# Optimization experiments

Measured on AMD Instinct MI355X. Metric: run time of the kernel, lower is better.

Reference implementation:

```python
import jax, jax.numpy as jnp
import numpy as np

N_SAMPLES = 2 ** 15          # 32768
STEP = 256                   # transform_step_size
WIN = 2048                   # transform/synthesis window
N_FRAMES = N_SAMPLES // STEP # 128
N_COEFFS = WIN // 2 + 1      # 1025
DILATIONS = (1, 2, 4, 8, 16, 32, 64, 1)


def hann(n):
    return 0.5 - 0.5 * jnp.cos(2.0 * jnp.pi * jnp.arange(n, dtype=jnp.float32) / n)


def transform(audio):
    # audio: (B, 1, N) -> magnitude STFT (B, 1024, 128)
    x = audio[:, 0, :]
    x = jnp.pad(x, ((0, 0), (0, WIN - STEP)))  # pad so n_frames == N_SAMPLES // STEP
    idx = np.arange(N_FRAMES)[:, None] * STEP + np.arange(WIN)[None, :]
    frames = x[:, idx] * hann(WIN)
    spec = jnp.abs(jnp.fft.rfft(frames, norm='ortho'))   # (B, F, 1025)
    return spec[..., : N_COEFFS - 1].transpose(0, 2, 1)  # (B, 1024, F)


def conv1x1(x, w, b):
    # x: (B, I, T), w: (O, I, 1), b: (O,)
    return jnp.einsum('oi,bit->bot', w[:, :, 0], x) + b[None, :, None]


def anticausal_block(x, w, b, dilation):
    # kernel_size=2 anti-causal dilated conv: looks at t and t+dilation (pad future)
    x_fut = jnp.pad(x, ((0, 0), (0, 0), (0, dilation)))[:, :, dilation:]
    y = (jnp.einsum('oi,bit->bot', w[:, :, 0], x)
         + jnp.einsum('oi,bit->bot', w[:, :, 1], x_fut)
         + b[None, :, None])
    y = jax.nn.leaky_relu(y, 0.2)
    y = y + x
    # do_norm: per-example max-norm
    y = y / (jnp.max(jnp.abs(y), axis=(1, 2), keepdims=True) + 1e-8)
    return y


def upsample_with_holes(x, desired_size):
    # zero-stuffing upsample: out[..., ::step] = x
    b, c, t = x.shape
    step = desired_size // t
    out = jnp.zeros((b, c, desired_size), x.dtype)
    return out.at[:, :, ::step].set(x)


def freq_domain_resonance(coeffs):
    # coeffs: (1, C, 1025) in [0, 1); per-frame decay = repeated spectral multiply
    c = jnp.clip(coeffs, 0.0, 0.9999)
    exps = jnp.arange(1, N_FRAMES + 1, dtype=coeffs.dtype)
    mags = c[:, :, None, :] ** exps[None, None, :, None]     # (1, C, F, 1025)
    frames = jnp.fft.irfft(mags, n=WIN) * hann(WIN)
    hop = WIN // 2
    total = hop * (N_FRAMES - 1) + WIN
    idx = np.arange(N_FRAMES)[:, None] * hop + np.arange(WIN)[None, :]
    out = jnp.zeros(frames.shape[:2] + (total,), frames.dtype)
    out = out.at[:, :, idx].add(frames)                      # overlap-add
    return out[..., :N_SAMPLES]                              # (1, C, N)


def fft_convolve(a, b):
    # circular-free conv via zero-padding to 2N, keep first N (matches repo fft_convolve)
    n = a.shape[-1]
    spec = jnp.fft.rfft(a, n=2 * n) * jnp.fft.rfft(b, n=2 * n)
    return jnp.fft.irfft(spec, n=2 * n)[..., :n]


def reference(audio, proj_in_w, proj_in_b, blocks_w, blocks_b,
              proj_sparse_w, proj_sparse_b, proj_dense_w, proj_dense_b, resonances):
    spec = transform(audio)                         # (B, 1024, 128)
    h = conv1x1(spec, proj_in_w, proj_in_b)         # (B, 32, 128)
    acc = jnp.zeros_like(h)
    for i, d in enumerate(DILATIONS):               # fixed 8-block stack
        h = anticausal_block(h, blocks_w[i], blocks_b[i], d)
        acc = acc + h
    x = conv1x1(acc, proj_sparse_w, proj_sparse_b)  # (B, 256, 128)
    sparse = jax.nn.relu(x)
    x = conv1x1(sparse, proj_dense_w, proj_dense_b) # (B, 32, 128)
    x = upsample_with_holes(x, N_SAMPLES)           # (B, 32, 32768)
    res = freq_domain_resonance(resonances)         # (1, 32, 32768), broadcast over B
    y = fft_convolve(x, res)                        # (B, 32, 32768)
    y = jnp.sum(y, axis=1, keepdims=True)           # (B, 1, 32768)
    return y, sparse


def setup_inputs() -> dict:
    key = jax.random.key(0)
    ks = jax.random.split(key, 12)
    u = lambda k, shape: jax.random.uniform(k, shape, jnp.float32, -0.05, 0.05)
    return {
        'audio': jax.random.normal(ks[0], (32, 1, N_SAMPLES), jnp.float32),
        'proj_in_w': u(ks[1], (32, 1024, 1)),
        'proj_in_b': jnp.zeros((32,), jnp.float32),
        'blocks_w': u(ks[2], (8, 32, 32, 2)),
        'blocks_b': jnp.zeros((8, 32), jnp.float32),
        'proj_sparse_w': u(ks[3], (256, 32, 1)),
        'proj_sparse_b': jnp.zeros((256,), jnp.float32),
        'proj_dense_w': u(ks[4], (32, 256, 1)),
        'proj_dense_b': jnp.zeros((32,), jnp.float32),
        'resonances': jax.random.uniform(ks[5], (1, 32, N_COEFFS), jnp.float32, 0.0, 1.0),
    }
```

## Files before the change

kernel.cpp:

```cpp
#include <hip/hip_runtime.h>

#define PI_F 3.14159265358979323846f

typedef short bf16x8 __attribute__((ext_vector_type(8)));
typedef float f32x4 __attribute__((ext_vector_type(4)));

#define MFMA16(acc, a, b) \
  acc = __builtin_amdgcn_mfma_f32_16x16x32_bf16(a, b, acc, 0, 0, 0)

#define WS_SPEC   0u
#define WS_H0     4194304u
#define WS_ACC    4325376u
#define WS_V      4456448u
#define WS_WTIN   4587520u
#define WS_WST    4620288u
#define WS_WDT    4628480u
#define WS_FRAMES 4636672u
#define WS_RES    6733824u

__device__ __forceinline__ void fft2048_stages(float2* buf, int tid) {
  for (int stage = 0; stage < 11; ++stage) {
    int half = 1 << stage;
    float base = -PI_F / (float)half;
    for (int t = tid; t < 1024; t += 256) {
      int j  = t & (half - 1);
      int i0 = ((t >> stage) << (stage + 1)) + j;
      int i1 = i0 + half;
      float s, c;
      __sincosf(base * (float)j, &s, &c);
      float2 u = buf[i0];
      float2 w = buf[i1];
      float tr = c * w.x - s * w.y;
      float ti = c * w.y + s * w.x;
      buf[i0] = make_float2(u.x + tr, u.y + ti);
      buf[i1] = make_float2(u.x - tr, u.y - ti);
    }
    __syncthreads();
  }
}

__global__ __launch_bounds__(256) void k_fft(const float* __restrict__ audio,
                                             const float* __restrict__ resin,
                                             float* __restrict__ spec,
                                             float* __restrict__ frames) {
  __shared__ float2 buf[2048];
  int blk = blockIdx.x;
  if (blk < 2048) {
    int b  = blk >> 6;
    int f0 = (blk & 63) * 2;
    for (int j = threadIdx.x; j < 2048; j += 256) {
      float h = 0.5f - 0.5f * __cosf(0.0030679615757712823f * (float)j);
      int i1 = f0 * 256 + j;
      int i2 = i1 + 256;
      float a1 = (i1 < 32768) ? audio[b * 32768 + i1] : 0.f;
      float a2 = (i2 < 32768) ? audio[b * 32768 + i2] : 0.f;
      buf[__brev((unsigned)j) >> 21] = make_float2(a1 * h, a2 * h);
    }
    __syncthreads();
    fft2048_stages(buf, threadIdx.x);
    const float scale = 0.5f * 0.022097086912079608f;
    for (int k = threadIdx.x; k < 1024; k += 256) {
      float2 zk = buf[k];
      float2 zn = buf[(2048 - k) & 2047];
      float f1r = zk.x + zn.x, f1i = zk.y - zn.y;
      float f2r = zk.y + zn.y, f2i = zk.x - zn.x;
      spec[(b * 128 + f0) * 1024 + k]     = sqrtf(f1r * f1r + f1i * f1i) * scale;
      spec[(b * 128 + f0 + 1) * 1024 + k] = sqrtf(f2r * f2r + f2i * f2i) * scale;
    }
  } else {
    int r = blk - 2048;
    int c = r >> 4;
    int g = r & 15;
    float e1 = (float)(2 * g + 1);
    for (int k = threadIdx.x; k < 2048; k += 256) {
      int kk = (k <= 1024) ? k : 2048 - k;
      float cv = resin[c * 1025 + kk];
      cv = fminf(fmaxf(cv, 0.f), 0.9999f);
      float m1 = __powf(cv, e1);
      float m2 = m1 * cv;
      buf[__brev((unsigned)k) >> 21] = make_float2(m1, m2);
    }
    __syncthreads();
    fft2048_stages(buf, threadIdx.x);
    for (int j = threadIdx.x; j < 2048; j += 256) {
      float h  = 0.5f - 0.5f * __cosf(0.0030679615757712823f * (float)j);
      float sc = h * (1.f / 2048.f);
      float2 z = buf[j];
      frames[(c * 32 + 2 * g) * 2048 + j]     = z.x * sc;
      frames[(c * 32 + 2 * g + 1) * 2048 + j] = z.y * sc;
    }
  }
}

__global__ __launch_bounds__(256) void k_prep(const float* __restrict__ Win,
                                              const float* __restrict__ Ws,
                                              const float* __restrict__ Wd,
                                              const float* __restrict__ bwIn,
                                              float* __restrict__ WT,
                                              float* __restrict__ WsT,
                                              float* __restrict__ WdT,
                                              short* __restrict__ Whg,
                                              short* __restrict__ Wlg) {
  int i = blockIdx.x * 256 + threadIdx.x;
  if (i < 32768) { int o = i >> 10, k = i & 1023; WT[k * 32 + o] = Win[i]; }
  if (i < 8192)  { int o2 = i >> 5, m = i & 31;   WsT[m * 256 + o2] = Ws[i]; }
  if (i < 8192)  { int c = i >> 8, o2 = i & 255;  WdT[o2 * 32 + c] = Wd[i]; }
  if (i < 16384) {
    int w = i & 1, m = (i >> 1) & 31, o = (i >> 6) & 31, s = i >> 11;
    float val = bwIn[i];
    unsigned bits = __float_as_uint(val);
    float rem = val - __uint_as_float(bits & 0xffff0000u);
    int row = (s * 2 + w) * 32 + o;
    Whg[row * 32 + m] = (short)(bits >> 16);
    Wlg[row * 32 + m] = (short)(__float_as_uint(rem) >> 16);
  }
}

__global__ __launch_bounds__(256) void k_proj_in(const float* __restrict__ spec,
                                                 const float* __restrict__ WT,
                                                 const float* __restrict__ bias,
                                                 float* __restrict__ h0) {
  __shared__ float specL[8][1024];
  __shared__ float red[32][8][8];
  int b  = blockIdx.x >> 4;
  int t0 = (blockIdx.x & 15) * 8;
  for (int i = threadIdx.x; i < 8192; i += 256) {
    int tt = i >> 10, k = i & 1023;
    specL[tt][k] = spec[(b * 128 + t0 + tt) * 1024 + k];
  }
  __syncthreads();
  int o = threadIdx.x & 31, p = threadIdx.x >> 5;
  float part[8] = {0.f,0.f,0.f,0.f,0.f,0.f,0.f,0.f};
  for (int i = 0; i < 128; ++i) {
    int k = p * 128 + ((i + p * 4) & 127);
    float w = WT[k * 32 + o];
#pragma unroll
    for (int tt = 0; tt < 8; ++tt) part[tt] += w * specL[tt][k];
  }
#pragma unroll
  for (int tt = 0; tt < 8; ++tt) red[o][tt][p] = part[tt];
  __syncthreads();
  int oo = threadIdx.x >> 3, tt2 = threadIdx.x & 7;
  float s = bias[oo];
#pragma unroll
  for (int p2 = 0; p2 < 8; ++p2) s += red[oo][tt2][p2];
  h0[b * 4096 + oo * 128 + t0 + tt2] = s;
}

__global__ __launch_bounds__(1024) void k_chain(const float* __restrict__ h0,
                                                const short* __restrict__ Whg,
                                                const short* __restrict__ Wlg,
                                                const float* __restrict__ bb,
                                                float* __restrict__ accout) {
  __shared__ __align__(16) short Hh[192 * 40];
  __shared__ __align__(16) short Hl[192 * 40];
  __shared__ float Hf[128 * 33];
  __shared__ float bL[256];
  __shared__ float red[16];
  int b = blockIdx.x, tid = threadIdx.x;

  for (int i = tid; i < 4096; i += 1024) {
    int t = i & 127;
    int o = i >> 7;
    float val = h0[b * 4096 + i];
    Hf[t * 33 + o] = val;
    unsigned bits = __float_as_uint(val);
    float rem = val - __uint_as_float(bits & 0xffff0000u);
    Hh[t * 40 + o] = (short)(bits >> 16);
    Hl[t * 40 + o] = (short)(__float_as_uint(rem) >> 16);
  }
  for (int i = tid; i < 64 * 40; i += 1024) {
    Hh[128 * 40 + i] = 0;
    Hl[128 * 40 + i] = 0;
  }
  if (tid < 256) bL[tid] = bb[tid];
  __syncthreads();

  int wave = tid >> 6, lane = tid & 63;
  int quad = lane >> 4, l15 = lane & 15;
  int t0 = (wave & 7) * 16, o0 = (wave >> 3) * 16;
  int tD = t0 + quad * 4;
  int oD = o0 + l15;

  const bf16x8* Hh8 = (const bf16x8*)Hh;
  const bf16x8* Hl8 = (const bf16x8*)Hl;
  const bf16x8* Wh8 = (const bf16x8*)Whg;
  const bf16x8* Wl8 = (const bf16x8*)Wlg;

  float accsum[4] = {0.f, 0.f, 0.f, 0.f};
  const int DIL[8] = {1, 2, 4, 8, 16, 32, 64, 1};

#pragma unroll
  for (int s = 0; s < 8; ++s) {
    int arow = t0 + l15;
    int frow = arow + DIL[s];
    bf16x8 Ah = Hh8[arow * 5 + quad];
    bf16x8 Al = Hl8[arow * 5 + quad];
    bf16x8 Fh = Hh8[frow * 5 + quad];
    bf16x8 Fl = Hl8[frow * 5 + quad];
    int w0row = ((s * 2 + 0) * 32 + oD) * 4 + quad;
    int w1row = ((s * 2 + 1) * 32 + oD) * 4 + quad;
    bf16x8 B0h = Wh8[w0row], B0l = Wl8[w0row];
    bf16x8 B1h = Wh8[w1row], B1l = Wl8[w1row];
    float bias = bL[s * 32 + oD];
    f32x4 acc = {bias, bias, bias, bias};
    MFMA16(acc, Ah, B0h); MFMA16(acc, Ah, B0l); MFMA16(acc, Al, B0h);
    MFMA16(acc, Fh, B1h); MFMA16(acc, Fh, B1l); MFMA16(acc, Fl, B1h);
    float hnew[4], lmax = 0.f;
#pragma unroll
    for (int r = 0; r < 4; ++r) {
      float sv = acc[r];
      sv = (sv > 0.f) ? sv : 0.2f * sv;
      sv += Hf[(tD + r) * 33 + oD];
      hnew[r] = sv;
      lmax = fmaxf(lmax, fabsf(sv));
    }
#pragma unroll
    for (int off = 32; off > 0; off >>= 1)
      lmax = fmaxf(lmax, __shfl_down(lmax, off, 64));
    if (lane == 0) red[wave] = lmax;
    __syncthreads();
    float mx = red[0];
#pragma unroll
    for (int i = 1; i < 16; ++i) mx = fmaxf(mx, red[i]);
    float nm = 1.f / (mx + 1e-8f);
#pragma unroll
    for (int r = 0; r < 4; ++r) {
      float hv = hnew[r] * nm;
      accsum[r] += hv;
      int t = tD + r;
      Hf[t * 33 + oD] = hv;
      unsigned bits = __float_as_uint(hv);
      float rem = hv - __uint_as_float(bits & 0xffff0000u);
      Hh[t * 40 + oD] = (short)(bits >> 16);
      Hl[t * 40 + oD] = (short)(__float_as_uint(rem) >> 16);
    }
    __syncthreads();
  }
#pragma unroll
  for (int r = 0; r < 4; ++r)
    accout[b * 4096 + (tD + r) * 32 + oD] = accsum[r];
}

__global__ __launch_bounds__(256) void k_sparse_dense(const float* __restrict__ acc,
                                                      const float* __restrict__ WsT,
                                                      const float* __restrict__ bs,
                                                      const float* __restrict__ WdT,
                                                      const float* __restrict__ bd,
                                                      float* __restrict__ out_sparse,
                                                      float* __restrict__ v) {
  __shared__ float accL[32];
  __shared__ float sL[256];
  __shared__ float red[8][32];
  int b = blockIdx.x >> 7, t = blockIdx.x & 127;
  int tid = threadIdx.x;
  if (tid < 32) accL[tid] = acc[b * 4096 + t * 32 + tid];
  __syncthreads();
  float s = bs[tid];
  for (int m = 0; m < 32; ++m) s += WsT[m * 256 + tid] * accL[m];
  s = fmaxf(s, 0.f);
  out_sparse[b * 32768 + tid * 128 + t] = s;
  sL[tid] = s;
  __syncthreads();
  int c = tid & 31, p = tid >> 5;
  float part = 0.f;
  for (int j = 0; j < 32; ++j) {
    int o2 = p * 32 + j;
    part += WdT[o2 * 32 + c] * sL[o2];
  }
  red[p][c] = part;
  __syncthreads();
  if (tid < 32) {
    float vv = bd[tid];
    for (int p2 = 0; p2 < 8; ++p2) vv += red[p2][tid];
    v[b * 4096 + tid * 128 + t] = vv;
  }
}

__global__ __launch_bounds__(256) void k_res_assemble(const float* __restrict__ frames,
                                                      float* __restrict__ res) {
  int i = blockIdx.x * 256 + threadIdx.x;
  int c = i >> 15, s = i & 32767;
  int g = s >> 10, j0 = s & 1023;
  float v = frames[(c * 32 + g) * 2048 + j0];
  if (g > 0) v += frames[(c * 32 + g - 1) * 2048 + j0 + 1024];
  res[i] = v;
}

__global__ __launch_bounds__(256) void k_bpack(const float* __restrict__ res,
                                               short* __restrict__ Bh,
                                               short* __restrict__ Bl) {
  int c = blockIdx.x >> 4, o = blockIdx.x & 15;
  int r = threadIdx.x;
  bf16x8 hv, lv;
#pragma unroll
  for (int j = 0; j < 8; ++j) {
    float val = res[c * 32768 + (8 * o + j) * 256 + r];
    unsigned bits = __float_as_uint(val);
    float rem = val - __uint_as_float(bits & 0xffff0000u);
    hv[j] = (short)(bits >> 16);
    lv[j] = (short)(__float_as_uint(rem) >> 16);
  }
  int unit = (blockIdx.x * 16 + (r >> 4)) * 16 + (r & 15);
  ((bf16x8*)Bh)[unit] = hv;
  ((bf16x8*)Bl)[unit] = lv;
}

__global__ __launch_bounds__(256) void k_conv(const float* __restrict__ v,
                                              const short* __restrict__ Bh,
                                              const short* __restrict__ Bl,
                                              float* __restrict__ y) {
  __shared__ float vwin[32][33];
  __shared__ __align__(16) short Ah[16 * 520];
  __shared__ __align__(16) short Al[16 * 520];
  int blk = blockIdx.x;
  int b = blk / 36;
  int p = blk - b * 36;
  int qt = (int)((sqrtf(8.f * (float)p + 1.f) - 1.f) * 0.5f + 1e-4f);
  int uc = p - ((qt * (qt + 1)) >> 1);
  int q0 = qt * 16, u0 = uc * 16;
  int D0 = q0 - u0;

  for (int i = threadIdx.x; i < 1024; i += 256) {
    int c = i >> 5, ii = i & 31;
    int d = D0 - 15 + ii;
    vwin[c][ii] = (d >= 0 && d < 128) ? v[b * 4096 + c * 128 + d] : 0.f;
  }
  __syncthreads();
  for (int idx = threadIdx.x; idx < 8192; idx += 256) {
    int m = idx >> 9, kk = idx & 511;
    float val = vwin[kk >> 4][(m - (kk & 15)) + 15];
    unsigned bits = __float_as_uint(val);
    float rem = val - __uint_as_float(bits & 0xffff0000u);
    Ah[m * 520 + kk] = (short)(bits >> 16);
    Al[m * 520 + kk] = (short)(__float_as_uint(rem) >> 16);
  }
  __syncthreads();

  int lane = threadIdx.x & 63, wave = threadIdx.x >> 6;
  int quad = lane >> 4, l15 = lane & 15;
  int nt0 = wave * 4;

  f32x4 acc[4];
#pragma unroll
  for (int i = 0; i < 4; ++i) acc[i] = (f32x4)0.f;

  const bf16x8* Ah8 = (const bf16x8*)Ah;
  const bf16x8* Al8 = (const bf16x8*)Al;
  const bf16x8* Bh8 = (const bf16x8*)Bh;
  const bf16x8* Bl8 = (const bf16x8*)Bl;
  int aoff = l15 * 65 + quad;
  int og   = 2 * uc + (quad & 1);
  int cq   = quad >> 1;

#pragma unroll
  for (int ks = 0; ks < 16; ++ks) {
    bf16x8 avh = Ah8[aoff + 4 * ks];
    bf16x8 avl = Al8[aoff + 4 * ks];
    int c = 2 * ks + cq;
    int bbase = (c * 16 + og) * 256 + l15;
#pragma unroll
    for (int t = 0; t < 4; ++t) {
      int bi = bbase + (nt0 + t) * 16;
      bf16x8 bvh = Bh8[bi];
      bf16x8 bvl = Bl8[bi];
      MFMA16(acc[t], avh, bvh);
      MFMA16(acc[t], avh, bvl);
      MFMA16(acc[t], avl, bvh);
    }
  }

  float* yb = y + b * 32768 + (q0 + quad * 4) * 256 + l15;
#pragma unroll
  for (int t = 0; t < 4; ++t)
#pragma unroll
    for (int reg = 0; reg < 4; ++reg)
      atomicAdd(yb + reg * 256 + (nt0 + t) * 16, acc[t][reg]);
}

extern "C" void kernel_launch(void* const* d_in, const int* in_sizes, int n_in,
                              void* d_out, int out_size, void* d_ws, size_t ws_size,
                              hipStream_t stream) {
  const float* audio = (const float*)d_in[0];
  const float* Win   = (const float*)d_in[1];
  const float* bin   = (const float*)d_in[2];
  const float* bw    = (const float*)d_in[3];
  const float* bb    = (const float*)d_in[4];
  const float* Ws    = (const float*)d_in[5];
  const float* bs    = (const float*)d_in[6];
  const float* Wd    = (const float*)d_in[7];
  const float* bd    = (const float*)d_in[8];
  const float* reson = (const float*)d_in[9];

  float* out = (float*)d_out;
  float* ws  = (float*)d_ws;

  float* spec   = ws + WS_SPEC;
  float* h0     = ws + WS_H0;
  float* accb   = ws + WS_ACC;
  float* vbuf   = ws + WS_V;
  float* WT     = ws + WS_WTIN;
  float* WsT    = ws + WS_WST;
  float* WdT    = ws + WS_WDT;
  float* frames = ws + WS_FRAMES;
  float* resbuf = ws + WS_RES;
  short* Bh = (short*)(ws + WS_FRAMES);
  short* Bl = (short*)(ws + WS_FRAMES + 524288u);
  short* Whg = (short*)(ws + WS_V);
  short* Wlg = (short*)(ws + WS_V + 8192u);

  hipMemsetAsync(d_out, 0, 1048576u * sizeof(float), stream);

  k_prep<<<128, 256, 0, stream>>>(Win, Ws, Wd, bw, WT, WsT, WdT, Whg, Wlg);
  k_fft<<<2560, 256, 0, stream>>>(audio, reson, spec, frames);
  k_res_assemble<<<4096, 256, 0, stream>>>(frames, resbuf);
  k_bpack<<<512, 256, 0, stream>>>(resbuf, Bh, Bl);
  k_proj_in<<<512, 256, 0, stream>>>(spec, WT, bin, h0);
  k_chain<<<32, 1024, 0, stream>>>(h0, Whg, Wlg, bb, accb);
  k_sparse_dense<<<4096, 256, 0, stream>>>(accb, WsT, bs, WdT, bd, out + 1048576, vbuf);
  k_conv<<<1152, 256, 0, stream>>>(vbuf, Bh, Bl, out);
}
```

Baseline: 209.3 us.

## Enlarge k_conv tiles to reuse B fragments across two batches and two row tiles

Rewrites the bf16-split MFMA convolution kernel so each block handles two batch items and a 32-row output tile, with four A sub-tiles sharing every loaded B fragment. Channels are processed in two passes through a smaller Toeplitz A buffer in LDS. This cuts global B traffic and the number of atomic-add blocks, shrinking the grid from 1152 to 320 blocks. In exchange it raises register pressure (16 accumulators) and may hurt occupancy and load balance on the triangular tile schedule.

```diff
diff --git a/kernel.cpp b/kernel.cpp
--- a/kernel.cpp
+++ b/kernel.cpp
@@ -306,76 +306,118 @@
   ((bf16x8*)Bl)[unit] = lv;
 }
 
-__global__ __launch_bounds__(256) void k_conv(const float* __restrict__ v,
-                                              const short* __restrict__ Bh,
-                                              const short* __restrict__ Bl,
-                                              float* __restrict__ y) {
-  __shared__ float vwin[32][33];
-  __shared__ __align__(16) short Ah[16 * 520];
-  __shared__ __align__(16) short Al[16 * 520];
+__global__ __launch_bounds__(256, 2) void k_conv(const float* __restrict__ v,
+                                                 const short* __restrict__ Bh,
+                                                 const short* __restrict__ Bl,
+                                                 float* __restrict__ y) {
+  __shared__ __align__(16) short AH[2 * 32 * 264];
+  __shared__ __align__(16) short AL[2 * 32 * 264];
+  __shared__ float vwin[2][2][16][48];
+
   int blk = blockIdx.x;
-  int b = blk / 36;
-  int p = blk - b * 36;
-  int qt = (int)((sqrtf(8.f * (float)p + 1.f) - 1.f) * 0.5f + 1e-4f);
-  int uc = p - ((qt * (qt + 1)) >> 1);
-  int q0 = qt * 16, u0 = uc * 16;
-  int D0 = q0 - u0;
-
-  for (int i = threadIdx.x; i < 1024; i += 256) {
-    int c = i >> 5, ii = i & 31;
-    int d = D0 - 15 + ii;
-    vwin[c][ii] = (d >= 0 && d < 128) ? v[b * 4096 + c * 128 + d] : 0.f;
-  }
-  __syncthreads();
-  for (int idx = threadIdx.x; idx < 8192; idx += 256) {
-    int m = idx >> 9, kk = idx & 511;
-    float val = vwin[kk >> 4][(m - (kk & 15)) + 15];
-    unsigned bits = __float_as_uint(val);
-    float rem = val - __uint_as_float(bits & 0xffff0000u);
-    Ah[m * 520 + kk] = (short)(bits >> 16);
-    Al[m * 520 + kk] = (short)(__float_as_uint(rem) >> 16);
+  int b2 = blk / 20;
+  int e  = blk - b2 * 20;
+  int j, uc;
+  if      (e < 2)  { j = 0; uc = e; }
+  else if (e < 6)  { j = 1; uc = e - 2; }
+  else if (e < 12) { j = 2; uc = e - 6; }
+  else             { j = 3; uc = e - 12; }
+  int D0 = 32 * j - 16 * uc;
+
+  for (int i = threadIdx.x; i < 3008; i += 256) {
+    int ii = i % 47;
+    int r  = i / 47;
+    int c  = r & 15, p = (r >> 4) & 1, bbv = r >> 5;
+    int d  = D0 - 15 + ii;
+    vwin[bbv][p][c][ii] = (d >= 0 && d < 128)
+        ? v[(2 * b2 + bbv) * 4096 + (16 * p + c) * 128 + d] : 0.f;
   }
   __syncthreads();
 
   int lane = threadIdx.x & 63, wave = threadIdx.x >> 6;
   int quad = lane >> 4, l15 = lane & 15;
-  int nt0 = wave * 4;
-
-  f32x4 acc[4];
-#pragma unroll
-  for (int i = 0; i < 4; ++i) acc[i] = (f32x4)0.f;
-
-  const bf16x8* Ah8 = (const bf16x8*)Ah;
-  const bf16x8* Al8 = (const bf16x8*)Al;
+  int cq   = quad >> 1;
+  int og   = 2 * uc + (quad & 1);
+  int nt0  = wave * 4;
+
+  f32x4 acc[4][4];
+#pragma unroll
+  for (int a = 0; a < 4; ++a)
+#pragma unroll
+    for (int t = 0; t < 4; ++t) acc[a][t] = (f32x4)0.f;
+
+  const bf16x8* AH8 = (const bf16x8*)AH;
+  const bf16x8* AL8 = (const bf16x8*)AL;
   const bf16x8* Bh8 = (const bf16x8*)Bh;
   const bf16x8* Bl8 = (const bf16x8*)Bl;
-  int aoff = l15 * 65 + quad;
-  int og   = 2 * uc + (quad & 1);
-  int cq   = quad >> 1;
-
-#pragma unroll
-  for (int ks = 0; ks < 16; ++ks) {
-    bf16x8 avh = Ah8[aoff + 4 * ks];
-    bf16x8 avl = Al8[aoff + 4 * ks];
-    int c = 2 * ks + cq;
-    int bbase = (c * 16 + og) * 256 + l15;
-#pragma unroll
-    for (int t = 0; t < 4; ++t) {
-      int bi = bbase + (nt0 + t) * 16;
-      bf16x8 bvh = Bh8[bi];
-      bf16x8 bvl = Bl8[bi];
-      MFMA16(acc[t], avh, bvh);
-      MFMA16(acc[t], avh, bvl);
-      MFMA16(acc[t], avl, bvh);
-    }
-  }
-
-  float* yb = y + b * 32768 + (q0 + quad * 4) * 256 + l15;
-#pragma unroll
-  for (int t = 0; t < 4; ++t)
-#pragma unroll
-    for (int reg = 0; reg < 4; ++reg)
-      atomicAdd(yb + reg * 256 + (nt0 + t) * 16, acc[t][reg]);
+  short2* AH2 = (short2*)AH;
+  short2* AL2 = (short2*)AL;
+
+  int abase[4];
+#pragma unroll
+  for (int bbi = 0; bbi < 2; ++bbi)
+#pragma unroll
+    for (int qs = 0; qs < 2; ++qs)
+      abase[bbi * 2 + qs] = (bbi * 32 + qs * 16 + l15) * 33 + quad;
+
+  for (int p = 0; p < 2; ++p) {
+    for (int i = threadIdx.x; i < 8192; i += 256) {
+      int kk2 = i & 127;
+      int row = (i >> 7) & 31;
+      int bbv = i >> 12;
+      int cl  = kk2 >> 3;
+      int uu  = (kk2 & 7) * 2;
+      int ii  = row - uu + 15;
+      float v0 = vwin[bbv][p][cl][ii];
+      float v1 = vwin[bbv][p][cl][ii - 1];
+      unsigned w0 = __float_as_uint(v0), w1 = __float_as_uint(v1);
+      float r0 = v0 - __uint_as_float(w0 & 0xffff0000u);
+      float r1 = v1 - __uint_as_float(w1 & 0xffff0000u);
+      int u2 = (bbv * 32 + row) * 132 + kk2;
+      AH2[u2] = make_short2((short)(w0 >> 16), (short)(w1 >> 16));
+      AL2[u2] = make_short2((short)(__float_as_uint(r0) >> 16),
+                            (short)(__float_as_uint(r1) >> 16));
+    }
+    __syncthreads();
+
+#pragma unroll
+    for (int ks = 0; ks < 8; ++ks) {
+      bf16x8 ah[4], al[4];
+#pragma unroll
+      for (int tl = 0; tl < 4; ++tl) {
+        ah[tl] = AH8[abase[tl] + ks * 4];
+        al[tl] = AL8[abase[tl] + ks * 4];
+      }
+      int c = 16 * p + 2 * ks + cq;
+      int bb0 = (c * 16 + og) * 256 + l15;
+#pragma unroll
+      for (int t = 0; t < 4; ++t) {
+        int bi = bb0 + (nt0 + t) * 16;
+        bf16x8 bvh = Bh8[bi];
+        bf16x8 bvl = Bl8[bi];
+#pragma unroll
+        for (int tl = 0; tl < 4; ++tl) {
+          MFMA16(acc[tl][t], ah[tl], bvh);
+          MFMA16(acc[tl][t], ah[tl], bvl);
+          MFMA16(acc[tl][t], al[tl], bvh);
+        }
+      }
+    }
+    __syncthreads();
+  }
+
+#pragma unroll
+  for (int bbi = 0; bbi < 2; ++bbi)
+#pragma unroll
+    for (int qs = 0; qs < 2; ++qs) {
+      float* yb = y + (2 * b2 + bbi) * 32768
+                    + (32 * j + qs * 16 + quad * 4) * 256 + l15;
+#pragma unroll
+      for (int t = 0; t < 4; ++t)
+#pragma unroll
+        for (int reg = 0; reg < 4; ++reg)
+          atomicAdd(yb + reg * 256 + (nt0 + t) * 16, acc[bbi * 2 + qs][t][reg]);
+    }
 }
 
 extern "C" void kernel_launch(void* const* d_in, const int* in_sizes, int n_in,
@@ -418,5 +460,5 @@
   k_proj_in<<<512, 256, 0, stream>>>(spec, WT, bin, h0);
   k_chain<<<32, 1024, 0, stream>>>(h0, Whg, Wlg, bb, accb);
   k_sparse_dense<<<4096, 256, 0, stream>>>(accb, WsT, bs, WdT, bd, out + 1048576, vbuf);
-  k_conv<<<1152, 256, 0, stream>>>(vbuf, Bh, Bl, out);
-}
+  k_conv<<<320, 256, 0, stream>>>(vbuf, Bh, Bl, out);
+}
```

Result: slower. 215.2 us (+2.8%).
